# Kernel tuning notes

Hardware: AMD Instinct MI355X
Metric: run time of the kernel (lower is better)

The kernel has to match this reference:

```python
import jax, jax.numpy as jnp
import numpy as np

DIM_EMB = 1024
NUM_HEADS = 16
DIM_HEAD = DIM_EMB // NUM_HEADS  # 64


def setup_inputs() -> dict:
    key = jax.random.key(0)
    k1, k2, k3 = jax.random.split(key, 3)
    x = jax.random.normal(k1, (4, 2048, DIM_EMB), dtype=jnp.float32)
    # nn.Linear(dim_embedding, 3*h*d, bias=False): weight shape [out, in]
    w_qkv = jax.random.normal(k2, (3 * NUM_HEADS * DIM_HEAD, DIM_EMB), dtype=jnp.float32) * (DIM_EMB ** -0.5)
    w_out = jax.random.normal(k3, (DIM_EMB, NUM_HEADS * DIM_HEAD), dtype=jnp.float32) * ((NUM_HEADS * DIM_HEAD) ** -0.5)
    return {"x": x, "w_qkv": w_qkv, "w_out": w_out}


def reference(x, w_qkv, w_out):
    b, t, _ = x.shape
    scale = DIM_HEAD ** -0.5
    qkv = jnp.einsum('bte,fe->btf', x, w_qkv)  # [b, t, 3*h*d]
    qkv = qkv.reshape(b, t, 3, NUM_HEADS, DIM_HEAD)  # fused dim order (k h d)
    q, k, v = qkv[:, :, 0], qkv[:, :, 1], qkv[:, :, 2]  # each [b, t, h, d]
    scores = jnp.einsum('bihd,bjhd->bhij', q, k) * scale  # [b, h, t, t]
    weights = jax.nn.softmax(scores, axis=-1)
    attn = jnp.einsum('bhij,bjhd->bhid', weights, v)  # [b, h, t, d]
    concat = attn.transpose(0, 2, 1, 3).reshape(b, t, NUM_HEADS * DIM_HEAD)
    return jnp.einsum('btf,ef->bte', concat, w_out)
```

## Files before the change

kernel.cpp:

```cpp
#include <hip/hip_runtime.h>

#define DI __device__ __forceinline__

typedef float  f32x2  __attribute__((ext_vector_type(2)));
typedef float  f32x4  __attribute__((ext_vector_type(4)));
typedef float  f32x16 __attribute__((ext_vector_type(16)));
typedef __bf16 bf16x8 __attribute__((ext_vector_type(8)));
typedef unsigned u32x2 __attribute__((ext_vector_type(2)));
typedef unsigned u32x4 __attribute__((ext_vector_type(4)));

static constexpr int TB   = 2048;
static constexpr int NTOK = 8192;
static constexpr int EMB  = 1024;
static constexpr int FQKV = 3072;

DI unsigned short f2bf(float f) {
  union { float f; unsigned u; } v; v.f = f;
  unsigned r = v.u + 0x7FFFu + ((v.u >> 16) & 1u);
  return (unsigned short)(r >> 16);
}

DI unsigned pack2bf(float a, float b) {
#if __has_builtin(__builtin_amdgcn_cvt_pk_bf16_f32)
  typedef __bf16 bf16x2 __attribute__((ext_vector_type(2)));
  bf16x2 r = __builtin_amdgcn_cvt_pk_bf16_f32(a, b);
  return __builtin_bit_cast(unsigned, r);
#else
  unsigned ua = __builtin_bit_cast(unsigned, a) + 0x8000u;
  unsigned ub = __builtin_bit_cast(unsigned, b) + 0x8000u;
  return __builtin_amdgcn_perm(ub, ua, 0x07060302u);
#endif
}

DI void plswap(unsigned& a, unsigned& b) {
#if __has_builtin(__builtin_amdgcn_permlane32_swap)
  u32x2 r = __builtin_amdgcn_permlane32_swap(a, b, false, false);
  a = r.x; b = r.y;
#else
  const bool hi = (threadIdx.x & 32) != 0;
  unsigned ax = (unsigned)__shfl_xor((int)a, 32);
  unsigned bx = (unsigned)__shfl_xor((int)b, 32);
  unsigned na = hi ? bx : a;
  unsigned nb = hi ? b : ax;
  a = na; b = nb;
#endif
}

DI bf16x8 frag4(unsigned a, unsigned b, unsigned c, unsigned d) {
  u32x4 u = {a, b, c, d};
  return __builtin_bit_cast(bf16x8, u);
}

DI void gload16(const void* g, void* l) {
  __builtin_amdgcn_global_load_lds(
      (__attribute__((address_space(1))) void*)(g),
      (__attribute__((address_space(3))) void*)(l), 16, 0, 0);
}

DI void wait_vm4() { asm volatile("s_waitcnt vmcnt(4)" ::: "memory"); }
DI void wait_vm0() { asm volatile("s_waitcnt vmcnt(0)" ::: "memory"); }
DI void rbar()     { __builtin_amdgcn_s_barrier(); }
DI void sfence()   { __builtin_amdgcn_sched_barrier(0); }

DI void syncdrain() {
  __builtin_amdgcn_s_waitcnt(0);
  __syncthreads();
}

__global__ __launch_bounds__(256)
void cvt_kernel(const float4* __restrict__ x, const float4* __restrict__ wq,
                const float4* __restrict__ wo,
                ushort4* __restrict__ xb, ushort4* __restrict__ wqb,
                ushort4* __restrict__ wob) {
  const int nx   = NTOK * EMB / 4;
  const int nq   = FQKV * EMB / 4;
  const int ntot = nx + nq + EMB * EMB / 4;
  for (int i = blockIdx.x * 256 + threadIdx.x; i < ntot; i += gridDim.x * 256) {
    float4 v; ushort4* dst;
    if (i < nx)           { v = x[i];            dst = xb  + i; }
    else if (i < nx + nq) { v = wq[i - nx];      dst = wqb + (i - nx); }
    else                  { v = wo[i - nx - nq]; dst = wob + (i - nx - nq); }
    ushort4 p;
    p.x = f2bf(v.x); p.y = f2bf(v.y); p.z = f2bf(v.z); p.w = f2bf(v.w);
    *dst = p;
  }
}

__global__ __launch_bounds__(512, 4)
void gemm_qkv(const unsigned short* __restrict__ A,
              const unsigned short* __restrict__ Bt,
              const int K,
              unsigned short* __restrict__ qk,
              unsigned short* __restrict__ vT) {
  __shared__ unsigned short sA[256 * 32];
  __shared__ unsigned short sB[128 * 32];
  const int tid  = threadIdx.x;
  const int w    = tid >> 6;
  const int l    = tid & 63;
  const int quad = l >> 4;
  const int lr   = l & 15;
  const int nwg  = gridDim.x * gridDim.y;
  const int orig = blockIdx.y * gridDim.x + blockIdx.x;
  const int swzb = (orig & 7) * (nwg >> 3) + (orig >> 3);
  const int n0   = (swzb % gridDim.x) * 128;
  const int m0   = (swzb / gridDim.x) * 256;
  const int wm   = (w >> 1) * 64;
  const int wn   = (w & 1) * 64;

  f32x4 acc[4][4];
#pragma unroll
  for (int i = 0; i < 4; ++i)
#pragma unroll
    for (int j = 0; j < 4; ++j) acc[i][j] = {0.f, 0.f, 0.f, 0.f};

  const int srow = l >> 2;
  const int sg   = (l & 3) ^ ((l >> 3) & 3);
  const unsigned short* gA = A  + (long)(m0 + w * 32 + srow) * K + sg * 8;
  const unsigned short* gB = Bt + (long)(n0 + w * 16 + srow) * K + sg * 8;
  unsigned short* lA = sA + w * 1024;
  unsigned short* lB = sB + w * 512;
  const int swz = (lr >> 1) & 3;

  for (int k0 = 0; k0 < K; k0 += 32) {
    gload16(gA + k0,          lA);
    gload16(gA + k0 + 16 * K, lA + 512);
    gload16(gB + k0,          lB);
    syncdrain();
    bf16x8 af[4], bfr[4];
#pragma unroll
    for (int rt = 0; rt < 4; ++rt)
      af[rt] = *(const bf16x8*)(sA + (wm + rt * 16 + lr) * 32 + (quad ^ swz) * 8);
#pragma unroll
    for (int ct = 0; ct < 4; ++ct)
      bfr[ct] = *(const bf16x8*)(sB + (wn + ct * 16 + lr) * 32 + (quad ^ swz) * 8);
#pragma unroll
    for (int rt = 0; rt < 4; ++rt)
#pragma unroll
      for (int ct = 0; ct < 4; ++ct)
        acc[rt][ct] = __builtin_amdgcn_mfma_f32_16x16x32_bf16(af[rt], bfr[ct],
                                                              acc[rt][ct], 0, 0, 0);
    __syncthreads();
  }

  if (n0 < 2048) {
    const float qs = (n0 < 1024) ? 0.18033688011112042f : 1.0f;
#pragma unroll
    for (int rt = 0; rt < 4; ++rt) {
      const int row = m0 + wm + rt * 16 + quad * 4;
#pragma unroll
      for (int ct = 0; ct < 4; ++ct) {
        const int col = n0 + wn + ct * 16 + lr;
#pragma unroll
        for (int r = 0; r < 4; ++r)
          qk[(long)(row + r) * 2048 + col] = f2bf(acc[rt][ct][r] * qs);
      }
    }
  } else {
#pragma unroll
    for (int rt = 0; rt < 4; ++rt) {
      const int tok = m0 + wm + rt * 16 + quad * 4;
      const int bb  = tok >> 11, tt = tok & 2047;
#pragma unroll
      for (int ct = 0; ct < 4; ++ct) {
        const int fv = n0 - 2048 + wn + ct * 16 + lr;
        ushort4 p;
        p.x = f2bf(acc[rt][ct][0]); p.y = f2bf(acc[rt][ct][1]);
        p.z = f2bf(acc[rt][ct][2]); p.w = f2bf(acc[rt][ct][3]);
        *(ushort4*)(vT + ((long)(bb * 1024 + fv)) * 2048 + tt) = p;
      }
    }
  }
}

__global__ __launch_bounds__(256, 4)
void gemm_out(const unsigned short* __restrict__ A,
              const unsigned short* __restrict__ Bt,
              const int K,
              float* __restrict__ outp) {
  __shared__ unsigned short sA[128 * 32];
  __shared__ unsigned short sB[64 * 32];
  const int tid  = threadIdx.x;
  const int w    = tid >> 6;
  const int l    = tid & 63;
  const int quad = l >> 4;
  const int lr   = l & 15;
  const int nwg  = gridDim.x * gridDim.y;
  const int orig = blockIdx.y * gridDim.x + blockIdx.x;
  const int swzb = (orig & 7) * (nwg >> 3) + (orig >> 3);
  const int n0   = (swzb % gridDim.x) * 64;
  const int m0   = (swzb / gridDim.x) * 128;
  const int wm   = (w >> 1) * 64;
  const int wn   = (w & 1) * 32;

  f32x4 acc[4][2];
#pragma unroll
  for (int i = 0; i < 4; ++i)
#pragma unroll
    for (int j = 0; j < 2; ++j) acc[i][j] = {0.f, 0.f, 0.f, 0.f};

  const int srow = l >> 2;
  const int sg   = (l & 3) ^ ((l >> 3) & 3);
  const unsigned short* gA = A  + (long)(m0 + w * 32 + srow) * K + sg * 8;
  const unsigned short* gB = Bt + (long)(n0 + w * 16 + srow) * K + sg * 8;
  unsigned short* lA = sA + w * 1024;
  unsigned short* lB = sB + w * 512;
  const int swz = (lr >> 1) & 3;

  for (int k0 = 0; k0 < K; k0 += 32) {
    gload16(gA + k0,          lA);
    gload16(gA + k0 + 16 * K, lA + 512);
    gload16(gB + k0,          lB);
    syncdrain();
    bf16x8 af[4], bfr[2];
#pragma unroll
    for (int rt = 0; rt < 4; ++rt)
      af[rt] = *(const bf16x8*)(sA + (wm + rt * 16 + lr) * 32 + (quad ^ swz) * 8);
#pragma unroll
    for (int ct = 0; ct < 2; ++ct)
      bfr[ct] = *(const bf16x8*)(sB + (wn + ct * 16 + lr) * 32 + (quad ^ swz) * 8);
#pragma unroll
    for (int rt = 0; rt < 4; ++rt)
#pragma unroll
      for (int ct = 0; ct < 2; ++ct)
        acc[rt][ct] = __builtin_amdgcn_mfma_f32_16x16x32_bf16(af[rt], bfr[ct],
                                                              acc[rt][ct], 0, 0, 0);
    __syncthreads();
  }

#pragma unroll
  for (int rt = 0; rt < 4; ++rt) {
    const int row = m0 + wm + rt * 16 + quad * 4;
#pragma unroll
    for (int ct = 0; ct < 2; ++ct) {
      const int col = n0 + wn + ct * 16 + lr;
#pragma unroll
      for (int r = 0; r < 4; ++r)
        outp[(long)(row + r) * 1024 + col] = acc[rt][ct][r];
    }
  }
}

__global__ __launch_bounds__(256, 4)
void attn_kernel(const unsigned short* __restrict__ qk,
                 const unsigned short* __restrict__ vT,
                 unsigned short* __restrict__ attnb) {
  __shared__ unsigned short sK[2][64 * 64];
  __shared__ unsigned short sV[2][64 * 64];
  const int tid = threadIdx.x;
  const int w   = tid >> 6;
  const int l   = tid & 63;
  const int l31 = l & 31;
  const int lh  = l >> 5;
  const int h8  = lh * 8;
  const int bh  = blockIdx.x;
  const int hh  = bh & 15;
  const long tokbase = (long)(bh >> 4) * TB;
  const int qbase = blockIdx.y * 128 + w * 32;

  bf16x8 qf[4];
  {
    const unsigned short* qptr = qk + (tokbase + qbase + l31) * 2048 + hh * 64 + h8;
#pragma unroll
    for (int s = 0; s < 4; ++s) qf[s] = *(const bf16x8*)(qptr + s * 16);
  }

  const int srow = l >> 3;
  const int g    = (l & 7) ^ srow;
  const unsigned short* kbase =
      qk + (tokbase + w * 16 + srow) * 2048 + 1024 + hh * 64 + g * 8;
  const unsigned short* vbase =
      vT + ((long)bh * 64 + w * 16 + srow) * 2048 + g * 8;

  f32x16 oacc[2] = {{}, {}};
  f32x2 lp2 = {0.f, 0.f};

  gload16(kbase,            &sK[0][(w * 16 + 0) * 64]);
  gload16(kbase + 8 * 2048, &sK[0][(w * 16 + 8) * 64]);
  gload16(vbase,            &sV[0][(w * 16 + 0) * 64]);
  gload16(vbase + 8 * 2048, &sV[0][(w * 16 + 8) * 64]);

  for (int t = 0; t < 32; ++t) {
    const int buf = t & 1;
    if (t + 1 < 32) {
      const int k0 = (t + 1) * 64;
      const int nb = buf ^ 1;
      gload16(kbase + (long)k0 * 2048,            &sK[nb][(w * 16 + 0) * 64]);
      gload16(kbase + (long)k0 * 2048 + 8 * 2048, &sK[nb][(w * 16 + 8) * 64]);
      gload16(vbase + k0,                         &sV[nb][(w * 16 + 0) * 64]);
      gload16(vbase + k0 + 8 * 2048,              &sV[nb][(w * 16 + 8) * 64]);
      wait_vm4();
    } else {
      wait_vm0();
    }
    sfence();
    rbar();
    sfence();
    const unsigned short* bK = sK[buf];
    const unsigned short* bV = sV[buf];

#pragma unroll
    for (int G = 0; G < 2; ++G) {
      f32x16 sacc = {};
      __builtin_amdgcn_s_setprio(1);
#pragma unroll
      for (int s = 0; s < 4; ++s) {
        const int key = G * 32 + l31;
        const int p   = (s * 2 + lh) ^ (key & 7);
        const bf16x8 kf = *(const bf16x8*)(bK + key * 64 + p * 8);
        sacc = __builtin_amdgcn_mfma_f32_32x32x16_bf16(kf, qf[s], sacc, 0, 0, 0);
      }
      __builtin_amdgcn_s_setprio(0);
      float e[16];
#pragma unroll
      for (int i = 0; i < 16; ++i) e[i] = __builtin_amdgcn_exp2f(sacc[i]);
#pragma unroll
      for (int i = 0; i < 8; ++i) {
        f32x2 pr = {e[2 * i], e[2 * i + 1]};
        lp2 += pr;
      }
      unsigned d[8];
#pragma unroll
      for (int i = 0; i < 8; ++i) d[i] = pack2bf(e[2 * i], e[2 * i + 1]);
      plswap(d[0], d[2]); plswap(d[1], d[3]);
      plswap(d[4], d[6]); plswap(d[5], d[7]);
      bf16x8 pp[2];
      pp[0] = frag4(d[0], d[1], d[2], d[3]);
      pp[1] = frag4(d[4], d[5], d[6], d[7]);
      __builtin_amdgcn_s_setprio(1);
#pragma unroll
      for (int sub = 0; sub < 2; ++sub) {
        const int gt  = (G * 2 + sub) * 2 + lh;
        const int d0r = l31, d1r = 32 + l31;
        const bf16x8 vf0 = *(const bf16x8*)(bV + d0r * 64 + ((gt ^ (d0r & 7))) * 8);
        const bf16x8 vf1 = *(const bf16x8*)(bV + d1r * 64 + ((gt ^ (d1r & 7))) * 8);
        oacc[0] = __builtin_amdgcn_mfma_f32_32x32x16_bf16(pp[sub], vf0, oacc[0], 0, 0, 0);
        oacc[1] = __builtin_amdgcn_mfma_f32_32x32x16_bf16(pp[sub], vf1, oacc[1], 0, 0, 0);
      }
      __builtin_amdgcn_s_setprio(0);
    }
    sfence();
    rbar();
  }

  const float lp = lp2.x + lp2.y;
  const float fs = lp + __shfl_xor(lp, 32);
  const float rc = 1.0f / fs;
#pragma unroll
  for (int r = 0; r < 16; ++r) {
    const int row = (r & 3) + 8 * (r >> 2) + 4 * lh;
    const float sc = __shfl(rc, row);
    const long base = (tokbase + qbase + row) * 1024 + hh * 64;
    attnb[base + l31]      = f2bf(oacc[0][r] * sc);
    attnb[base + 32 + l31] = f2bf(oacc[1][r] * sc);
  }
}

extern "C" void kernel_launch(void* const* d_in, const int* in_sizes, int n_in,
                              void* d_out, int out_size, void* d_ws, size_t ws_size,
                              hipStream_t stream) {
  const float* x    = (const float*)d_in[0];
  const float* wqkv = (const float*)d_in[1];
  const float* wout = (const float*)d_in[2];
  float* outp = (float*)d_out;

  unsigned short* xb    = (unsigned short*)d_ws;
  unsigned short* wqkvb = xb    + (long)NTOK * EMB;
  unsigned short* woutb = wqkvb + (long)FQKV * EMB;
  unsigned short* qkb   = woutb + (long)EMB * EMB;
  unsigned short* vTb   = qkb   + (long)NTOK * 2048;
  unsigned short* attnb = vTb   + (long)4 * 16 * 64 * TB;

  cvt_kernel<<<3072, 256, 0, stream>>>(
      (const float4*)x, (const float4*)wqkv, (const float4*)wout,
      (ushort4*)xb, (ushort4*)wqkvb, (ushort4*)woutb);

  gemm_qkv<<<dim3(24, 32), 512, 0, stream>>>(xb, wqkvb, EMB, qkb, vTb);

  attn_kernel<<<dim3(64, 16), 256, 0, stream>>>(qkb, vTb, attnb);

  gemm_out<<<dim3(16, 64), 256, 0, stream>>>(attnb, woutb, EMB, outp);
}
```

Measured before the change: 266.6 us.

## Rewrite QKV GEMM with 256x256 tiles and double-buffered async LDS pipeline

Replaces the QKV projection GEMM with a 256x256 tile kernel that uses a K-step of 64. It double-buffers LDS and issues global-to-LDS loads for the next tiles while MFMAs run over eight sub-phases per iteration, raising MFMA priority with s_setprio. The goal is to hide the per-K-step load-and-drain stall of the old single-buffered 256x128 kernel and to improve operand reuse. In exchange it uses more LDS and registers (launch bound drops to 2 blocks per CU) and launches fewer workgroups (384), which may leave CUs underfilled.

Result: slower. 315.9 us (+18.5%).

```diff
diff --git a/kernel.cpp b/kernel.cpp
--- a/kernel.cpp
+++ b/kernel.cpp
@@ -59,6 +59,7 @@
 
 DI void wait_vm4() { asm volatile("s_waitcnt vmcnt(4)" ::: "memory"); }
 DI void wait_vm0() { asm volatile("s_waitcnt vmcnt(0)" ::: "memory"); }
+DI void wait_lgkm0() { asm volatile("s_waitcnt lgkmcnt(0)" ::: "memory"); }
 DI void rbar()     { __builtin_amdgcn_s_barrier(); }
 DI void sfence()   { __builtin_amdgcn_sched_barrier(0); }
 
@@ -86,14 +87,14 @@
   }
 }
 
-__global__ __launch_bounds__(512, 4)
-void gemm_qkv(const unsigned short* __restrict__ A,
-              const unsigned short* __restrict__ Bt,
-              const int K,
-              unsigned short* __restrict__ qk,
-              unsigned short* __restrict__ vT) {
-  __shared__ unsigned short sA[256 * 32];
-  __shared__ unsigned short sB[128 * 32];
+__global__ __launch_bounds__(512, 2)
+void gemm_qkv8(const unsigned short* __restrict__ A,
+               const unsigned short* __restrict__ Bt,
+               const int K,
+               unsigned short* __restrict__ qk,
+               unsigned short* __restrict__ vT) {
+  __shared__ unsigned short sA[2][256 * 64];
+  __shared__ unsigned short sB[2][256 * 64];
   const int tid  = threadIdx.x;
   const int w    = tid >> 6;
   const int l    = tid & 63;
@@ -101,71 +102,143 @@
   const int lr   = l & 15;
   const int nwg  = gridDim.x * gridDim.y;
   const int orig = blockIdx.y * gridDim.x + blockIdx.x;
-  const int swzb = (orig & 7) * (nwg >> 3) + (orig >> 3);
-  const int n0   = (swzb % gridDim.x) * 128;
-  const int m0   = (swzb / gridDim.x) * 256;
-  const int wm   = (w >> 1) * 64;
-  const int wn   = (w & 1) * 64;
-
-  f32x4 acc[4][4];
-#pragma unroll
-  for (int i = 0; i < 4; ++i)
+  const int swz  = (orig & 7) * (nwg >> 3) + (orig >> 3);
+  const int n0   = (swz % gridDim.x) * 256;
+  const int m0   = (swz / gridDim.x) * 256;
+  const int wm   = (w >> 2) * 128;
+  const int wn   = (w & 3) * 64;
+
+  f32x4 acc[8][4];
+#pragma unroll
+  for (int i = 0; i < 8; ++i)
 #pragma unroll
     for (int j = 0; j < 4; ++j) acc[i][j] = {0.f, 0.f, 0.f, 0.f};
 
-  const int srow = l >> 2;
-  const int sg   = (l & 3) ^ ((l >> 3) & 3);
-  const unsigned short* gA = A  + (long)(m0 + w * 32 + srow) * K + sg * 8;
-  const unsigned short* gB = Bt + (long)(n0 + w * 16 + srow) * K + sg * 8;
-  unsigned short* lA = sA + w * 1024;
-  unsigned short* lB = sB + w * 512;
-  const int swz = (lr >> 1) & 3;
-
-  for (int k0 = 0; k0 < K; k0 += 32) {
-    gload16(gA + k0,          lA);
-    gload16(gA + k0 + 16 * K, lA + 512);
-    gload16(gB + k0,          lB);
-    syncdrain();
-    bf16x8 af[4], bfr[4];
-#pragma unroll
-    for (int rt = 0; rt < 4; ++rt)
-      af[rt] = *(const bf16x8*)(sA + (wm + rt * 16 + lr) * 32 + (quad ^ swz) * 8);
-#pragma unroll
-    for (int ct = 0; ct < 4; ++ct)
-      bfr[ct] = *(const bf16x8*)(sB + (wn + ct * 16 + lr) * 32 + (quad ^ swz) * 8);
-#pragma unroll
-    for (int rt = 0; rt < 4; ++rt)
-#pragma unroll
-      for (int ct = 0; ct < 4; ++ct)
-        acc[rt][ct] = __builtin_amdgcn_mfma_f32_16x16x32_bf16(af[rt], bfr[ct],
-                                                              acc[rt][ct], 0, 0, 0);
-    __syncthreads();
-  }
+  const int srow8 = l >> 3;
+  const int gsw   = ((l & 7) ^ srow8) * 8;
+  int rA[2][2], rB[2][2];
+#pragma unroll
+  for (int h = 0; h < 2; ++h)
+#pragma unroll
+    for (int jj = 0; jj < 2; ++jj) {
+      const int q0 = w * 16 + jj * 8;
+      rA[h][jj] = ((q0 >> 6) << 7) + h * 64 + (q0 & 63);
+      rB[h][jj] = ((q0 >> 5) << 6) + h * 32 + (q0 & 31);
+    }
+  const unsigned short* gAp[2][2];
+  const unsigned short* gBp[2][2];
+  int ldsA[2][2], ldsB[2][2];
+#pragma unroll
+  for (int h = 0; h < 2; ++h)
+#pragma unroll
+    for (int jj = 0; jj < 2; ++jj) {
+      gAp[h][jj] = A  + (long)(m0 + rA[h][jj] + srow8) * K + gsw;
+      gBp[h][jj] = Bt + (long)(n0 + rB[h][jj] + srow8) * K + gsw;
+      ldsA[h][jj] = rA[h][jj] * 64;
+      ldsB[h][jj] = rB[h][jj] * 64;
+    }
+
+  const int NT  = K >> 6;
+  const int NIT = NT >> 1;
+
+#define SG_A(buf, t, h)                                                 \
+  do {                                                                  \
+    gload16(gAp[h][0] + (t) * 64, &sA[buf][ldsA[h][0]]);                \
+    gload16(gAp[h][1] + (t) * 64, &sA[buf][ldsA[h][1]]);                \
+  } while (0)
+#define SG_B(buf, t, h)                                                 \
+  do {                                                                  \
+    gload16(gBp[h][0] + (t) * 64, &sB[buf][ldsB[h][0]]);                \
+    gload16(gBp[h][1] + (t) * 64, &sB[buf][ldsB[h][1]]);                \
+  } while (0)
+
+  SG_A(0, 0, 0); SG_B(0, 0, 0); SG_A(0, 0, 1); SG_B(0, 0, 1);
+  SG_A(1, 1, 0); SG_B(1, 1, 0);
+  wait_vm4();
+  sfence();
+  rbar();
+  sfence();
+
+#define PHASE(bufi, mh, nh, STG, WAITC)                                      \
+    do {                                                                     \
+      STG;                                                                   \
+      bf16x8 afr[4][2], bfr[2][2];                                           \
+      const unsigned short* aS = &sA[bufi][0];                               \
+      const unsigned short* bS = &sB[bufi][0];                               \
+      _Pragma("unroll")                                                      \
+      for (int ks = 0; ks < 2; ++ks) {                                       \
+        _Pragma("unroll")                                                    \
+        for (int nf = 0; nf < 2; ++nf) {                                     \
+          const int r = wn + (nh) * 32 + nf * 16 + lr;                       \
+          bfr[nf][ks] = *(const bf16x8*)(bS + r * 64 +                       \
+                          (((ks * 4 + quad) ^ (r & 7)) * 8));                \
+        }                                                                    \
+        _Pragma("unroll")                                                    \
+        for (int m = 0; m < 4; ++m) {                                        \
+          const int ra = wm + (mh) * 64 + m * 16 + lr;                       \
+          afr[m][ks] = *(const bf16x8*)(aS + ra * 64 +                       \
+                          (((ks * 4 + quad) ^ (ra & 7)) * 8));               \
+        }                                                                    \
+      }                                                                      \
+      rbar();                                                                \
+      wait_lgkm0();                                                          \
+      sfence();                                                              \
+      __builtin_amdgcn_s_setprio(1);                                         \
+      _Pragma("unroll")                                                      \
+      for (int m = 0; m < 4; ++m)                                            \
+        _Pragma("unroll")                                                    \
+        for (int nf = 0; nf < 2; ++nf)                                       \
+          _Pragma("unroll")                                                  \
+          for (int ks = 0; ks < 2; ++ks)                                     \
+            acc[(mh) * 4 + m][(nh) * 2 + nf] =                               \
+                __builtin_amdgcn_mfma_f32_16x16x32_bf16(                     \
+                    afr[m][ks], bfr[nf][ks],                                 \
+                    acc[(mh) * 4 + m][(nh) * 2 + nf], 0, 0, 0);              \
+      __builtin_amdgcn_s_setprio(0);                                         \
+      WAITC;                                                                 \
+      rbar();                                                                \
+    } while (0)
+
+  for (int j = 0; j < NIT; ++j) {
+    const int e = 2 * j, o = 2 * j + 1;
+    const bool s2 = (e + 2 < NT);
+    PHASE(0, 0, 0, SG_A(1, o, 1), );
+    PHASE(0, 0, 1, SG_B(1, o, 1), );
+    PHASE(0, 1, 0, if (s2) SG_A(0, e + 2, 0), );
+    PHASE(0, 1, 1, if (s2) SG_B(0, e + 2, 0), if (s2) wait_vm4(); else wait_vm0(););
+    PHASE(1, 0, 0, if (s2) SG_A(0, e + 2, 1), );
+    PHASE(1, 0, 1, if (s2) SG_B(0, e + 2, 1), );
+    PHASE(1, 1, 0, if (s2) SG_A(1, o + 2, 0), );
+    PHASE(1, 1, 1, if (s2) SG_B(1, o + 2, 0), if (s2) wait_vm4(););
+  }
+#undef PHASE
+#undef SG_A
+#undef SG_B
 
   if (n0 < 2048) {
     const float qs = (n0 < 1024) ? 0.18033688011112042f : 1.0f;
 #pragma unroll
-    for (int rt = 0; rt < 4; ++rt) {
-      const int row = m0 + wm + rt * 16 + quad * 4;
-#pragma unroll
-      for (int ct = 0; ct < 4; ++ct) {
-        const int col = n0 + wn + ct * 16 + lr;
+    for (int m = 0; m < 8; ++m) {
+      const int row = m0 + wm + m * 16 + quad * 4;
+#pragma unroll
+      for (int nf = 0; nf < 4; ++nf) {
+        const int col = n0 + wn + nf * 16 + lr;
 #pragma unroll
         for (int r = 0; r < 4; ++r)
-          qk[(long)(row + r) * 2048 + col] = f2bf(acc[rt][ct][r] * qs);
+          qk[(long)(row + r) * 2048 + col] = f2bf(acc[m][nf][r] * qs);
       }
     }
   } else {
 #pragma unroll
-    for (int rt = 0; rt < 4; ++rt) {
-      const int tok = m0 + wm + rt * 16 + quad * 4;
+    for (int m = 0; m < 8; ++m) {
+      const int tok = m0 + wm + m * 16 + quad * 4;
       const int bb  = tok >> 11, tt = tok & 2047;
 #pragma unroll
-      for (int ct = 0; ct < 4; ++ct) {
-        const int fv = n0 - 2048 + wn + ct * 16 + lr;
+      for (int nf = 0; nf < 4; ++nf) {
+        const int fv = n0 - 2048 + wn + nf * 16 + lr;
         ushort4 p;
-        p.x = f2bf(acc[rt][ct][0]); p.y = f2bf(acc[rt][ct][1]);
-        p.z = f2bf(acc[rt][ct][2]); p.w = f2bf(acc[rt][ct][3]);
+        p.x = f2bf(acc[m][nf][0]); p.y = f2bf(acc[m][nf][1]);
+        p.z = f2bf(acc[m][nf][2]); p.w = f2bf(acc[m][nf][3]);
         *(ushort4*)(vT + ((long)(bb * 1024 + fv)) * 2048 + tt) = p;
       }
     }
@@ -374,7 +447,7 @@
       (const float4*)x, (const float4*)wqkv, (const float4*)wout,
       (ushort4*)xb, (ushort4*)wqkvb, (ushort4*)woutb);
 
-  gemm_qkv<<<dim3(24, 32), 512, 0, stream>>>(xb, wqkvb, EMB, qkb, vTb);
+  gemm_qkv8<<<dim3(12, 32), 512, 0, stream>>>(xb, wqkvb, EMB, qkb, vTb);
 
   attn_kernel<<<dim3(64, 16), 256, 0, stream>>>(qkb, vTb, attnb);
 
```
